# Performance work log

Measured on AMD Instinct MI355X. Metric: run time of the kernel, lower is better.

Reference implementation:

```python
import jax, jax.numpy as jnp
import numpy as np

IN, H, T, B, HW = 2048, 512, 14, 256, 49

def setup_inputs() -> dict:
    key = jax.random.key(0)
    ks = jax.random.split(key, 10)
    s = 0.02
    return {
        "x": jax.random.normal(ks[0], (B, IN, HW), jnp.float32),
        "fixation": jax.random.randint(ks[1], (B, T), 0, HW, jnp.int64),
        # stacked gate weights, order: 0=input, 1=forget, 2=output, 3=memory
        "Wx": jax.random.normal(ks[2], (4, H, IN), jnp.float32) * s,
        "bx": jnp.zeros((4, H), jnp.float32),
        "Wh": jax.random.normal(ks[3], (4, H, H), jnp.float32) * s,
        "bh": jnp.zeros((4, H), jnp.float32),
        # peephole weights, order: 0=input_c, 1=forget_c, 2=output_c
        "Wc": jax.random.normal(ks[4], (3, H, H), jnp.float32) * s,
        "bc": jnp.zeros((3, H), jnp.float32),
        "Wd": jax.random.normal(ks[5], (1, H), jnp.float32) * s,
        "bd": jnp.zeros((1,), jnp.float32),
    }

def reference(x, fixation, Wx, bx, Wh, bh, Wc, bc, Wd, bd):
    batch, feat, hw = x.shape
    seq_len = fixation.shape[1]
    # process_lengths: padding token is index 0
    lengths = seq_len - jnp.sum(fixation == 0, axis=1)  # [B]
    # gather fixated feature columns: [B, feat, T] -> [B, T, feat]
    xg = jnp.take_along_axis(x, fixation[:, None, :], axis=2)
    xg = jnp.transpose(xg, (0, 2, 1))
    # precompute all input projections for all 4 gates: [B, T, 4, H]
    xproj = jnp.einsum('btf,ghf->btgh', xg, Wx) + bx

    def step(carry, xp):  # xp: [B, 4, H]
        h, c = carry
        hp = jnp.einsum('bk,ghk->bgh', h, Wh) + bh  # [B, 4, H]
        i = jax.nn.sigmoid(xp[:, 0] + hp[:, 0] + c @ Wc[0].T + bc[0])
        f = jax.nn.sigmoid(xp[:, 1] + hp[:, 1] + c @ Wc[1].T + bc[1])
        g = jnp.tanh(xp[:, 3] + hp[:, 3])
        next_c = f * c + i * g
        o = jax.nn.sigmoid(xp[:, 2] + hp[:, 2] + next_c @ Wc[2].T + bc[2])
        h = o * next_c
        return (h, next_c), h

    hidden = Wx.shape[1]
    init = (jnp.zeros((batch, hidden), x.dtype), jnp.zeros((batch, hidden), x.dtype))
    _, hs = jax.lax.scan(step, init, jnp.transpose(xproj, (1, 0, 2, 3)))  # [T, B, H]
    hs = jnp.transpose(hs, (1, 0, 2))  # [B, T, H]
    # crop_seq: select hidden at end of each valid sequence
    last = hs[jnp.arange(batch), lengths - 1]  # [B, H]
    return jax.nn.sigmoid(last @ Wd.T + bd)  # [B, 1]
```

## Files before the change

### kernel.cpp

```cpp
#include <hip/hip_runtime.h>
#include <cstdint>
#include <cstddef>

#define B_   256
#define T_   14
#define INF_ 2048
#define H_   512
#define HW_  49
#define NG_  2048
#define KC_  1024
#define NBLK 256

typedef __attribute__((ext_vector_type(8))) _Float16 f16x8;
typedef __attribute__((ext_vector_type(4))) float f32x4;
typedef _Float16 f16;

typedef const void __attribute__((address_space(1))) gvoid_t;
typedef void __attribute__((address_space(3))) svoid_t;

__device__ __forceinline__ void async16(const void* g, void* l) {
  __builtin_amdgcn_global_load_lds((gvoid_t*)g, (svoid_t*)l, 16, 0, 0);
}

__device__ __forceinline__ float sigm(float x) { return 1.0f / (1.0f + __expf(-x)); }

__device__ __forceinline__ float aload(const float* p) {
  return __hip_atomic_load(p, __ATOMIC_RELAXED, __HIP_MEMORY_SCOPE_AGENT);
}
__device__ __forceinline__ unsigned long long aload64(const void* p) {
  return __hip_atomic_load((const unsigned long long*)p, __ATOMIC_RELAXED, __HIP_MEMORY_SCOPE_AGENT);
}
__device__ __forceinline__ void astore(float* p, float v) {
  __hip_atomic_store(p, v, __ATOMIC_RELAXED, __HIP_MEMORY_SCOPE_AGENT);
}
__device__ __forceinline__ void astore32(void* p, unsigned v) {
  __hip_atomic_store((unsigned*)p, v, __ATOMIC_RELAXED, __HIP_MEMORY_SCOPE_AGENT);
}

__device__ __forceinline__ void waitSlots(const int* slots, const int target) {
  const int* p = slots + (threadIdx.x & 31);
  for (;;) {
    const int v = __hip_atomic_load(p, __ATOMIC_RELAXED, __HIP_MEMORY_SCOPE_AGENT);
    if (__all(v >= target)) break;
    __builtin_amdgcn_s_sleep(1);
  }
}

__global__ void k_prep(const float* __restrict__ Wx, const float* __restrict__ bx,
                       const float* __restrict__ Wh, const float* __restrict__ Wc,
                       const float* __restrict__ bh, const float* __restrict__ bc,
                       const int* __restrict__ fix,
                       f16* __restrict__ Wxh, float* __restrict__ bxp,
                       f16* __restrict__ Wbig, f16* __restrict__ Wc2h,
                       float* __restrict__ biasb, int* __restrict__ flag64)
{
  __shared__ int any;
  const int tid = blockIdx.x * blockDim.x + threadIdx.x;
  const int nth = gridDim.x * blockDim.x;
  if (blockIdx.x == 0) {
    if (threadIdx.x == 0) any = 0;
    __syncthreads();
    int a = 0;
    for (int j = 1 + 2 * (int)threadIdx.x; j < B_ * T_; j += 2 * (int)blockDim.x) a |= fix[j];
    if (a) any = 1;
    __syncthreads();
    if (threadIdx.x == 0) flag64[0] = (any == 0) ? 1 : 0;
  }
  for (int i = tid; i < 4 * H_ * INF_; i += nth) {
    const int n = i >> 11, k = i & 2047;
    const int g = n & 3, h = n >> 2;
    Wxh[i] = (f16)Wx[((size_t)(g * H_ + h)) * INF_ + k];
  }
  for (int i = tid; i < NG_ * KC_; i += nth) {
    const int n = i >> 10, k = i & 1023;
    const int g = n & 3, h = n >> 2;
    float v;
    if (k < H_) v = Wh[((size_t)(g * H_ + h)) * H_ + k];
    else {
      const int kk = k - H_;
      v = (g == 0) ? Wc[h * H_ + kk] : (g == 1) ? Wc[H_ * H_ + h * H_ + kk] : 0.0f;
    }
    Wbig[i] = (f16)v;
  }
  for (int i = tid; i < H_ * H_; i += nth) Wc2h[i] = (f16)Wc[2 * H_ * H_ + i];
  for (int i = tid; i < NG_; i += nth) {
    const int g = i & 3, h = i >> 2;
    biasb[i] = bh[g * H_ + h] + ((g == 0) ? bc[h] : (g == 1) ? bc[H_ + h] : 0.0f);
    bxp[i] = bx[g * H_ + h];
  }
}

__global__ __launch_bounds__(256) void k_gather(const float* __restrict__ x,
                                                const int* __restrict__ fix,
                                                const int* __restrict__ flag64,
                                                f16* __restrict__ xg,
                                                int* __restrict__ tlast)
{
  __shared__ float rows[256 * 49];
  __shared__ int wv[T_];
  const int b = blockIdx.x;
  const int tid = threadIdx.x;
  const int is64 = flag64[0];
  if (tid < T_) wv[tid] = is64 ? fix[2 * (b * T_ + tid)] : fix[b * T_ + tid];
  __syncthreads();
  if (blockIdx.y == 0 && tid == 0) {
    int cnt = 0;
    for (int t = 0; t < T_; ++t) cnt += (wv[t] == 0);
    tlast[b] = (cnt < T_) ? (T_ - 1 - cnt) : (T_ - 1);
  }
  const float* xb = x + (size_t)b * (INF_ * HW_);
  for (int c = 0; c < 2; ++c) {
    const int ch = blockIdx.y * 2 + c;
    if (c) __syncthreads();
    const float4* src = (const float4*)(xb + (size_t)ch * 256 * 49);
    float4* dst4 = (float4*)rows;
    for (int i = tid; i < 3136; i += 256) dst4[i] = src[i];
    __syncthreads();
#pragma unroll
    for (int t = 0; t < T_; ++t)
      xg[(size_t)(b * T_ + t) * INF_ + ch * 256 + tid] = (f16)rows[tid * 49 + wv[t]];
  }
}

__global__ __launch_bounds__(256) void k_gemm_big(
    const f16* __restrict__ A, const f16* __restrict__ Bw,
    const float* __restrict__ bxp, float* __restrict__ Cproj)
{
  __shared__ alignas(16) f16 As[128 * 64];
  __shared__ alignas(16) f16 Bs[128 * 64];
  const int tid = threadIdx.x;
  const int lane = tid & 63;
  const int w = tid >> 6;
  const int wm = w >> 1, wn = w & 1;
  const int flat = blockIdx.y * 16 + blockIdx.x;
  const int wg = (flat & 7) * 56 + (flat >> 3);
  const int m0 = (wg >> 4) * 128, n0 = (wg & 15) * 128;
  f32x4 acc[4][4] = {};
  const int lrow = lane >> 3;
  const int kg = lane & 7;
  for (int ks = 0; ks < 2048; ks += 64) {
#pragma unroll
    for (int q = 0; q < 4; ++q) {
      const int chunk = (w << 2) + q;
      const int row = (chunk << 3) + lrow;
      const int skg = kg ^ (row & 7);
      async16(A + (size_t)(m0 + row) * 2048 + ks + (skg << 3), As + chunk * 512);
      async16(Bw + (size_t)(n0 + row) * 2048 + ks + (skg << 3), Bs + chunk * 512);
    }
    __syncthreads();
#pragma unroll
    for (int kk = 0; kk < 2; ++kk) {
      const int kgl = (kk << 2) + (lane >> 4);
      f16x8 af[4], bf[4];
#pragma unroll
      for (int mi = 0; mi < 4; ++mi) {
        const int r = (wm << 6) + (mi << 4) + (lane & 15);
        af[mi] = *(const f16x8*)(As + r * 64 + ((kgl ^ (r & 7)) << 3));
      }
#pragma unroll
      for (int ni = 0; ni < 4; ++ni) {
        const int r = (wn << 6) + (ni << 4) + (lane & 15);
        bf[ni] = *(const f16x8*)(Bs + r * 64 + ((kgl ^ (r & 7)) << 3));
      }
#pragma unroll
      for (int mi = 0; mi < 4; ++mi)
#pragma unroll
        for (int ni = 0; ni < 4; ++ni)
          acc[mi][ni] = __builtin_amdgcn_mfma_f32_16x16x32_f16(af[mi], bf[ni], acc[mi][ni], 0, 0, 0);
    }
    __syncthreads();
  }
#pragma unroll
  for (int mi = 0; mi < 4; ++mi)
#pragma unroll
    for (int ni = 0; ni < 4; ++ni)
#pragma unroll
      for (int r4 = 0; r4 < 4; ++r4) {
        const int row = m0 + (wm << 6) + (mi << 4) + ((lane >> 4) << 2) + r4;
        const int col = n0 + (wn << 6) + (ni << 4) + (lane & 15);
        Cproj[(size_t)row * 2048 + col] = acc[mi][ni][r4] + bxp[col];
      }
}

__global__ __launch_bounds__(256, 1) void k_recur(
    const f16* __restrict__ Wbig, const f16* __restrict__ Wc2h,
    const float* __restrict__ biasb, const float* __restrict__ bc,
    const float* __restrict__ xproj, f16* __restrict__ h16,
    f16* __restrict__ cb16, float* __restrict__ lasth,
    const int* __restrict__ tlast, const float* __restrict__ Wd,
    const float* __restrict__ bd, float* __restrict__ out,
    int* __restrict__ bar)
{
  __shared__ alignas(16) f16 hT[2][16 * 512];
  __shared__ alignas(16) f16 cT[2][16 * 512];
  __shared__ alignas(16) float exCN[256];
  __shared__ alignas(16) float exGO[2][256];
  __shared__ alignas(16) float ex2[4 * 256];
  const int tid = threadIdx.x, lane = tid & 63, w = tid >> 6;
  const int lk = lane >> 4;
  const int bid = blockIdx.x;
  const int pair = bid >> 5, grank = bid & 31;
  const int n0A = grank * 64, n0h = grank * 16;
  const int m0t[2] = {pair * 32, pair * 32 + 16};
  int* const sl[2] = {bar + (2 * pair) * 64, bar + (2 * pair + 1) * 64};

  f16x8 wG[32];
  {
    const f16* src = Wbig + (size_t)(n0A + w * 16 + (lane & 15)) * 1024 + (lk << 3);
#pragma unroll
    for (int kc = 0; kc < 32; ++kc) wG[kc] = *(const f16x8*)(src + kc * 32);
  }
  f16x8 wO[4];
  {
    const f16* src = Wc2h + (size_t)(n0h + (lane & 15)) * 512 + (lk << 3);
#pragma unroll
    for (int j = 0; j < 4; ++j) wO[j] = *(const f16x8*)(src + (w * 4 + j) * 32);
  }
  const int hq = (lane >> 2) & 3;
  const int browA = (lk << 2) + (lane & 3);
  const int hlA = w * 4 + hq;
  const float4 b4c = *(const float4*)(biasb + 4 * (n0h + hlA));
  const int rowB = tid >> 4, colB = tid & 15;
  const float bco = bc[1024 + n0h + colB];
  const int tlB[2] = {tlast[m0t[0] + rowB], tlast[m0t[1] + rowB]};
  {
    const f16x8 z = {};
#pragma unroll
    for (int j = 0; j < 8; ++j) *(f16x8*)(&cT[0][0] + (((j << 8) + tid) << 3)) = z;
  }
  float creg[2] = {0.f, 0.f};
  __syncthreads();

  for (int t = 0; t < T_; ++t) {
    float4 x4p[2];
#pragma unroll
    for (int tt = 0; tt < 2; ++tt)
      x4p[tt] = *(const float4*)(xproj + (size_t)((m0t[tt] + browA) * T_ + t) * 2048 +
                                 4 * (n0h + hlA));

#pragma unroll
    for (int tt = 0; tt < 2; ++tt) {
      if (t) waitSlots(sl[tt], 2 * t);
#pragma unroll
      for (int j = 0; j < 4; ++j) {
        const int u = (j << 8) + tid;
        const int row = u >> 6, kg = u & 63;
        const f16* src = h16 + (size_t)(m0t[tt] + row) * 512 + (kg << 3);
        union { f16x8 v; unsigned long long q[2]; } u2;
        u2.q[0] = aload64(src);
        u2.q[1] = aload64(src + 4);
        *(f16x8*)(&hT[tt][0] + row * 512 + ((kg >> 3) << 6) + (((kg & 7) ^ (row & 7)) << 3)) = u2.v;
      }
      __syncthreads();
      f32x4 acc[2] = {};
      {
        const int ra = lane & 15;
#pragma unroll
        for (int kc = 0; kc < 32; ++kc) {
          const int kgl = ((kc & 1) << 2) + lk;
          const f16* base = (kc < 16) ? (&hT[tt][0] + ((kc >> 1) << 6))
                                      : (&cT[tt][0] + (((kc - 16) >> 1) << 6));
          const f16x8 af = *(const f16x8*)(base + ra * 512 + ((kgl ^ (ra & 7)) << 3));
          acc[kc & 1] = __builtin_amdgcn_mfma_f32_16x16x32_f16(af, wG[kc], acc[kc & 1], 0, 0, 0);
        }
      }
      {
        const f32x4 a = acc[0] + acc[1];
        float a0 = a[0], a1 = a[1], a2 = a[2], a3 = a[3];
        {
          const bool odd = lane & 1;
          float xx = odd ? a0 : a1, yy = odd ? a2 : a3;
          xx = __shfl_xor(xx, 1); yy = __shfl_xor(yy, 1);
          if (odd) { a0 = xx; a2 = yy; } else { a1 = xx; a3 = yy; }
        }
        {
          const bool hi = lane & 2;
          float xx = hi ? a0 : a2, yy = hi ? a1 : a3;
          xx = __shfl_xor(xx, 2); yy = __shfl_xor(yy, 2);
          if (hi) { a0 = xx; a1 = yy; } else { a2 = xx; a3 = yy; }
        }
        const float gi = a0 + b4c.x + x4p[tt].x;
        const float gf = a1 + b4c.y + x4p[tt].y;
        const float go = a2 + b4c.z + x4p[tt].z;
        const float gm = a3 + b4c.w + x4p[tt].w;
        const float cn = sigm(gi) * tanhf(gm) + sigm(gf) * creg[tt];
        creg[tt] = cn;
        exCN[browA * 16 + hlA] = cn;
        exGO[tt][browA * 16 + hlA] = go;
      }
      __syncthreads();
      if (tid < 128) {
        const int rowe = tid >> 3, pr = tid & 7;
        const float2 cp = *(const float2*)(exCN + rowe * 16 + (pr << 1));
        union { unsigned u; f16 h2[2]; } pk;
        pk.h2[0] = (f16)cp.x; pk.h2[1] = (f16)cp.y;
        astore32(cb16 + (size_t)(m0t[tt] + rowe) * 512 + n0h + (pr << 1), pk.u);
      }
      __syncthreads();
      if (tid == 0)
        __hip_atomic_store(sl[tt] + grank, 2 * t + 1, __ATOMIC_RELAXED, __HIP_MEMORY_SCOPE_AGENT);
    }

#pragma unroll
    for (int tt = 0; tt < 2; ++tt) {
      waitSlots(sl[tt], 2 * t + 1);
#pragma unroll
      for (int j = 0; j < 4; ++j) {
        const int u = (j << 8) + tid;
        const int row = u >> 6, kg = u & 63;
        const f16* src = cb16 + (size_t)(m0t[tt] + row) * 512 + (kg << 3);
        union { f16x8 v; unsigned long long q[2]; } u2;
        u2.q[0] = aload64(src);
        u2.q[1] = aload64(src + 4);
        *(f16x8*)(&cT[tt][0] + row * 512 + ((kg >> 3) << 6) + (((kg & 7) ^ (row & 7)) << 3)) = u2.v;
      }
      __syncthreads();
      f32x4 accB = {};
      {
        const int ra = lane & 15;
#pragma unroll
        for (int j = 0; j < 4; ++j) {
          const int kc = w * 4 + j;
          const int kgl = ((kc & 1) << 2) + lk;
          const f16x8 af = *(const f16x8*)(&cT[tt][0] + ra * 512 + ((kc >> 1) << 6) +
                                           ((kgl ^ (ra & 7)) << 3));
          accB = __builtin_amdgcn_mfma_f32_16x16x32_f16(af, wO[j], accB, 0, 0, 0);
        }
      }
#pragma unroll
      for (int r4 = 0; r4 < 4; ++r4)
        ex2[w * 256 + ((lk << 2) + r4) * 16 + (lane & 15)] = accB[r4];
      __syncthreads();
      {
        const int ib = rowB * 16 + colB;
        const float sum = (ex2[ib] + ex2[256 + ib]) + (ex2[512 + ib] + ex2[768 + ib]);
        const int cg = n0h + colB;
        const float cn = (float)cT[tt][rowB * 512 + ((cg >> 6) << 6) +
                                       ((((cg >> 3) & 7) ^ (rowB & 7)) << 3) + (cg & 7)];
        const float hv = sigm(sum + exGO[tt][ib] + bco) * cn;
        const float hvo = __shfl_xor(hv, 1);
        if (!(tid & 1)) {
          union { unsigned u; f16 h2[2]; } pk;
          pk.h2[0] = (f16)hv; pk.h2[1] = (f16)hvo;
          astore32(h16 + (size_t)(m0t[tt] + rowB) * 512 + (cg & ~1), pk.u);
        }
        if (t == tlB[tt]) astore(lasth + (size_t)(m0t[tt] + rowB) * 512 + cg, hv);
      }
      __syncthreads();
      if (tid == 0)
        __hip_atomic_store(sl[tt] + grank, 2 * t + 2, __ATOMIC_RELAXED, __HIP_MEMORY_SCOPE_AGENT);
    }
  }

  waitSlots(sl[0], 2 * T_);
  waitSlots(sl[1], 2 * T_);
  if (w == 0) {
    const int b = pair * 32 + grank;
    float s = 0.f;
#pragma unroll
    for (int k = lane; k < 512; k += 64) s += aload(lasth + (size_t)b * 512 + k) * Wd[k];
#pragma unroll
    for (int off = 32; off > 0; off >>= 1) s += __shfl_down(s, off);
    if (lane == 0) out[b] = 1.0f / (1.0f + __expf(-(s + bd[0])));
  }
}

extern "C" void kernel_launch(void* const* d_in, const int* in_sizes, int n_in,
                              void* d_out, int out_size, void* d_ws, size_t ws_size,
                              hipStream_t stream) {
  const float* x   = (const float*)d_in[0];
  const int*   fix = (const int*)d_in[1];
  const float* Wx  = (const float*)d_in[2];
  const float* bx  = (const float*)d_in[3];
  const float* Wh  = (const float*)d_in[4];
  const float* bh  = (const float*)d_in[5];
  const float* Wc  = (const float*)d_in[6];
  const float* bc  = (const float*)d_in[7];
  const float* Wd  = (const float*)d_in[8];
  const float* bd  = (const float*)d_in[9];
  float* out = (float*)d_out;
  char* ws = (char*)d_ws;

  f16*   xg    = (f16*)(ws);
  f16*   Wxh   = (f16*)(ws + 14680064);
  float* xproj = (float*)(ws + 23068672);
  f16*   Wbig  = (f16*)(ws + 52428800);
  f16*   Wc2h  = (f16*)(ws + 56623104);
  float* biasb = (float*)(ws + 57147392);
  float* bxp   = (float*)(ws + 57155584);
  f16*   h16   = (f16*)(ws + 57163776);
  f16*   cb16  = (f16*)(ws + 57425920);
  float* lasth = (float*)(ws + 57688064);
  int*   tlast = (int*)(ws + 58212352);
  int*   flag64= (int*)(ws + 58213376);
  int*   bar   = (int*)(ws + 58213440);

  hipMemsetAsync(h16, 0, 262144, stream);
  hipMemsetAsync(cb16, 0, 262144, stream);
  hipMemsetAsync(bar, 0, 4096, stream);

  k_prep<<<2048, 256, 0, stream>>>(Wx, bx, Wh, Wc, bh, bc, fix, Wxh, bxp, Wbig, Wc2h, biasb, flag64);
  k_gather<<<dim3(256, 4), 256, 0, stream>>>(x, fix, flag64, xg, tlast);
  k_gemm_big<<<dim3(16, 28), 256, 0, stream>>>(xg, Wxh, bxp, xproj);
  k_recur<<<NBLK, 256, 0, stream>>>(Wbig, Wc2h, biasb, bc, xproj, h16, cb16,
                                    lasth, tlast, Wd, bd, out, bar);
}
```

Baseline: 217.9 us.

## Merge prep and gather kernels, restructure recurrence sync and block grouping

Merges the weight-prep and gather kernels into one launch, where each gather block recomputes the int64 flag itself. In the recurrence kernel, block-to-group mapping changes so group members are strided across block IDs. The cell-state export is written straight from registers instead of being staged in shared memory. The output-gate GEMM now runs on a single wave, removing the cross-wave reduction and one barrier per substep. The spin-wait polls two flag copies (one stored with an sc0 store) without sleeping. This cuts barriers and launch overhead, but leaves three waves idle during the output step and adds busier polling traffic.

```diff
diff --git a/kernel.cpp b/kernel.cpp
--- a/kernel.cpp
+++ b/kernel.cpp
@@ -27,6 +27,9 @@
 __device__ __forceinline__ float aload(const float* p) {
   return __hip_atomic_load(p, __ATOMIC_RELAXED, __HIP_MEMORY_SCOPE_AGENT);
 }
+__device__ __forceinline__ int aloadi(const int* p) {
+  return __hip_atomic_load(p, __ATOMIC_RELAXED, __HIP_MEMORY_SCOPE_AGENT);
+}
 __device__ __forceinline__ unsigned long long aload64(const void* p) {
   return __hip_atomic_load((const unsigned long long*)p, __ATOMIC_RELAXED, __HIP_MEMORY_SCOPE_AGENT);
 }
@@ -36,89 +39,97 @@
 __device__ __forceinline__ void astore32(void* p, unsigned v) {
   __hip_atomic_store((unsigned*)p, v, __ATOMIC_RELAXED, __HIP_MEMORY_SCOPE_AGENT);
 }
-
-__device__ __forceinline__ void waitSlots(const int* slots, const int target) {
-  const int* p = slots + (threadIdx.x & 31);
+__device__ __forceinline__ void astorei(int* p, int v) {
+  __hip_atomic_store(p, v, __ATOMIC_RELAXED, __HIP_MEMORY_SCOPE_AGENT);
+}
+
+__device__ __forceinline__ void st32_sc0(void* p, unsigned v) {
+  asm volatile("global_store_dword %0, %1, off sc0" :: "v"(p), "v"(v) : "memory");
+}
+__device__ __forceinline__ int ld_sc0_probe(const int* p) {
+  int r;
+  asm volatile("global_load_dword %0, %1, off sc0\n\ts_waitcnt vmcnt(0)"
+               : "=v"(r) : "v"(p) : "memory");
+  return r;
+}
+
+__device__ __forceinline__ void waitDual(const int* sa, const int* sf, const int target) {
+  const int* pa = sa + (threadIdx.x & 31);
+  const int* pf = sf + (threadIdx.x & 31);
   for (;;) {
-    const int v = __hip_atomic_load(p, __ATOMIC_RELAXED, __HIP_MEMORY_SCOPE_AGENT);
-    if (__all(v >= target)) break;
-    __builtin_amdgcn_s_sleep(1);
-  }
-}
-
-__global__ void k_prep(const float* __restrict__ Wx, const float* __restrict__ bx,
-                       const float* __restrict__ Wh, const float* __restrict__ Wc,
-                       const float* __restrict__ bh, const float* __restrict__ bc,
-                       const int* __restrict__ fix,
-                       f16* __restrict__ Wxh, float* __restrict__ bxp,
-                       f16* __restrict__ Wbig, f16* __restrict__ Wc2h,
-                       float* __restrict__ biasb, int* __restrict__ flag64)
+    const int vf = ld_sc0_probe(pf);
+    const int va = aloadi(pa);
+    if (__all((vf >= target) || (va >= target))) break;
+  }
+}
+
+__global__ __launch_bounds__(256) void k_prep_gather(
+    const float* __restrict__ Wx, const float* __restrict__ bx,
+    const float* __restrict__ Wh, const float* __restrict__ Wc,
+    const float* __restrict__ bh, const float* __restrict__ bc,
+    const int* __restrict__ fix, const float* __restrict__ x,
+    f16* __restrict__ Wxh, float* __restrict__ bxp,
+    f16* __restrict__ Wbig, f16* __restrict__ Wc2h,
+    float* __restrict__ biasb, f16* __restrict__ xg, int* __restrict__ tlast)
 {
-  __shared__ int any;
-  const int tid = blockIdx.x * blockDim.x + threadIdx.x;
-  const int nth = gridDim.x * blockDim.x;
-  if (blockIdx.x == 0) {
-    if (threadIdx.x == 0) any = 0;
+  const int bid = blockIdx.x;
+  const int tid = threadIdx.x;
+  if (bid < 1024) {
+    __shared__ float rows[256 * 49];
+    __shared__ int wv[T_];
+    __shared__ int anyS;
+    const int b = bid >> 2, part = bid & 3;
+    int a = 0;
+    for (int i = tid; i < B_ * T_; i += 256) a |= fix[2 * i + 1];
+    if (tid == 0) anyS = 0;
     __syncthreads();
-    int a = 0;
-    for (int j = 1 + 2 * (int)threadIdx.x; j < B_ * T_; j += 2 * (int)blockDim.x) a |= fix[j];
-    if (a) any = 1;
+    if (a) anyS = 1;
     __syncthreads();
-    if (threadIdx.x == 0) flag64[0] = (any == 0) ? 1 : 0;
-  }
-  for (int i = tid; i < 4 * H_ * INF_; i += nth) {
-    const int n = i >> 11, k = i & 2047;
-    const int g = n & 3, h = n >> 2;
-    Wxh[i] = (f16)Wx[((size_t)(g * H_ + h)) * INF_ + k];
-  }
-  for (int i = tid; i < NG_ * KC_; i += nth) {
-    const int n = i >> 10, k = i & 1023;
-    const int g = n & 3, h = n >> 2;
-    float v;
-    if (k < H_) v = Wh[((size_t)(g * H_ + h)) * H_ + k];
-    else {
-      const int kk = k - H_;
-      v = (g == 0) ? Wc[h * H_ + kk] : (g == 1) ? Wc[H_ * H_ + h * H_ + kk] : 0.0f;
-    }
-    Wbig[i] = (f16)v;
-  }
-  for (int i = tid; i < H_ * H_; i += nth) Wc2h[i] = (f16)Wc[2 * H_ * H_ + i];
-  for (int i = tid; i < NG_; i += nth) {
-    const int g = i & 3, h = i >> 2;
-    biasb[i] = bh[g * H_ + h] + ((g == 0) ? bc[h] : (g == 1) ? bc[H_ + h] : 0.0f);
-    bxp[i] = bx[g * H_ + h];
-  }
-}
-
-__global__ __launch_bounds__(256) void k_gather(const float* __restrict__ x,
-                                                const int* __restrict__ fix,
-                                                const int* __restrict__ flag64,
-                                                f16* __restrict__ xg,
-                                                int* __restrict__ tlast)
-{
-  __shared__ float rows[256 * 49];
-  __shared__ int wv[T_];
-  const int b = blockIdx.x;
-  const int tid = threadIdx.x;
-  const int is64 = flag64[0];
-  if (tid < T_) wv[tid] = is64 ? fix[2 * (b * T_ + tid)] : fix[b * T_ + tid];
-  __syncthreads();
-  if (blockIdx.y == 0 && tid == 0) {
-    int cnt = 0;
-    for (int t = 0; t < T_; ++t) cnt += (wv[t] == 0);
-    tlast[b] = (cnt < T_) ? (T_ - 1 - cnt) : (T_ - 1);
-  }
-  const float* xb = x + (size_t)b * (INF_ * HW_);
-  for (int c = 0; c < 2; ++c) {
-    const int ch = blockIdx.y * 2 + c;
-    if (c) __syncthreads();
-    const float4* src = (const float4*)(xb + (size_t)ch * 256 * 49);
-    float4* dst4 = (float4*)rows;
-    for (int i = tid; i < 3136; i += 256) dst4[i] = src[i];
+    const int is64 = (anyS == 0);
+    if (tid < T_) wv[tid] = is64 ? fix[2 * (b * T_ + tid)] : fix[b * T_ + tid];
     __syncthreads();
-#pragma unroll
-    for (int t = 0; t < T_; ++t)
-      xg[(size_t)(b * T_ + t) * INF_ + ch * 256 + tid] = (f16)rows[tid * 49 + wv[t]];
+    if (part == 0 && tid == 0) {
+      int cnt = 0;
+      for (int t = 0; t < T_; ++t) cnt += (wv[t] == 0);
+      tlast[b] = (cnt < T_) ? (T_ - 1 - cnt) : (T_ - 1);
+    }
+    const float* xb = x + (size_t)b * (INF_ * HW_);
+    for (int c = 0; c < 2; ++c) {
+      const int ch = part * 2 + c;
+      if (c) __syncthreads();
+      const float4* src = (const float4*)(xb + (size_t)ch * 256 * 49);
+      float4* dst4 = (float4*)rows;
+      for (int i = tid; i < 3136; i += 256) dst4[i] = src[i];
+      __syncthreads();
+#pragma unroll
+      for (int t = 0; t < T_; ++t)
+        xg[(size_t)(b * T_ + t) * INF_ + ch * 256 + tid] = (f16)rows[tid * 49 + wv[t]];
+    }
+  } else {
+    const int tid2 = (bid - 1024) * 256 + tid;
+    const int nth = 512 * 256;
+    for (int i = tid2; i < 4 * H_ * INF_; i += nth) {
+      const int n = i >> 11, k = i & 2047;
+      const int g = n & 3, h = n >> 2;
+      Wxh[i] = (f16)Wx[((size_t)(g * H_ + h)) * INF_ + k];
+    }
+    for (int i = tid2; i < NG_ * KC_; i += nth) {
+      const int n = i >> 10, k = i & 1023;
+      const int g = n & 3, h = n >> 2;
+      float v;
+      if (k < H_) v = Wh[((size_t)(g * H_ + h)) * H_ + k];
+      else {
+        const int kk = k - H_;
+        v = (g == 0) ? Wc[h * H_ + kk] : (g == 1) ? Wc[H_ * H_ + h * H_ + kk] : 0.0f;
+      }
+      Wbig[i] = (f16)v;
+    }
+    for (int i = tid2; i < H_ * H_; i += nth) Wc2h[i] = (f16)Wc[2 * H_ * H_ + i];
+    for (int i = tid2; i < NG_; i += nth) {
+      const int g = i & 3, h = i >> 2;
+      biasb[i] = bh[g * H_ + h] + ((g == 0) ? bc[h] : (g == 1) ? bc[H_ + h] : 0.0f);
+      bxp[i] = bx[g * H_ + h];
+    }
   }
 }
 
@@ -193,16 +204,17 @@
 {
   __shared__ alignas(16) f16 hT[2][16 * 512];
   __shared__ alignas(16) f16 cT[2][16 * 512];
-  __shared__ alignas(16) float exCN[256];
   __shared__ alignas(16) float exGO[2][256];
-  __shared__ alignas(16) float ex2[4 * 256];
   const int tid = threadIdx.x, lane = tid & 63, w = tid >> 6;
   const int lk = lane >> 4;
   const int bid = blockIdx.x;
-  const int pair = bid >> 5, grank = bid & 31;
-  const int n0A = grank * 64, n0h = grank * 16;
-  const int m0t[2] = {pair * 32, pair * 32 + 16};
-  int* const sl[2] = {bar + (2 * pair) * 64, bar + (2 * pair + 1) * 64};
+  const int grp = bid & 7, rank = bid >> 3;
+  const int n0A = rank * 64, n0h = rank * 16;
+  const int m0t[2] = {grp * 32, grp * 32 + 16};
+  int* const slA0 = bar + (grp * 2) * 32;
+  int* const slA1 = bar + (grp * 2 + 1) * 32;
+  int* const slF0 = bar + 512 + (grp * 2) * 32;
+  int* const slF1 = bar + 512 + (grp * 2 + 1) * 32;
 
   f16x8 wG[32];
   {
@@ -210,19 +222,24 @@
 #pragma unroll
     for (int kc = 0; kc < 32; ++kc) wG[kc] = *(const f16x8*)(src + kc * 32);
   }
-  f16x8 wO[4];
-  {
+  f16x8 wO[16];
+  float bcoW = 0.f;
+  int tlW0[4] = {-1, -1, -1, -1}, tlW1[4] = {-1, -1, -1, -1};
+  if (w == 0) {
     const f16* src = Wc2h + (size_t)(n0h + (lane & 15)) * 512 + (lk << 3);
 #pragma unroll
-    for (int j = 0; j < 4; ++j) wO[j] = *(const f16x8*)(src + (w * 4 + j) * 32);
+    for (int kc = 0; kc < 16; ++kc) wO[kc] = *(const f16x8*)(src + kc * 32);
+    bcoW = bc[1024 + n0h + (lane & 15)];
+#pragma unroll
+    for (int r4 = 0; r4 < 4; ++r4) {
+      tlW0[r4] = tlast[m0t[0] + lk * 4 + r4];
+      tlW1[r4] = tlast[m0t[1] + lk * 4 + r4];
+    }
   }
   const int hq = (lane >> 2) & 3;
   const int browA = (lk << 2) + (lane & 3);
   const int hlA = w * 4 + hq;
   const float4 b4c = *(const float4*)(biasb + 4 * (n0h + hlA));
-  const int rowB = tid >> 4, colB = tid & 15;
-  const float bco = bc[1024 + n0h + colB];
-  const int tlB[2] = {tlast[m0t[0] + rowB], tlast[m0t[1] + rowB]};
   {
     const f16x8 z = {};
 #pragma unroll
@@ -232,6 +249,9 @@
   __syncthreads();
 
   for (int t = 0; t < T_; ++t) {
+#pragma unroll
+    for (int kc = 0; kc < 32; ++kc) asm volatile("" : "+v"(wG[kc]));
+
     float4 x4p[2];
 #pragma unroll
     for (int tt = 0; tt < 2; ++tt)
@@ -240,7 +260,9 @@
 
 #pragma unroll
     for (int tt = 0; tt < 2; ++tt) {
-      if (t) waitSlots(sl[tt], 2 * t);
+      int* const slA = tt ? slA1 : slA0;
+      int* const slF = tt ? slF1 : slF0;
+      if (t) waitDual(slA, slF, 2 * t);
 #pragma unroll
       for (int j = 0; j < 4; ++j) {
         const int u = (j << 8) + tid;
@@ -285,25 +307,27 @@
         const float gm = a3 + b4c.w + x4p[tt].w;
         const float cn = sigm(gi) * tanhf(gm) + sigm(gf) * creg[tt];
         creg[tt] = cn;
-        exCN[browA * 16 + hlA] = cn;
         exGO[tt][browA * 16 + hlA] = go;
-      }
+        const float cnP = __shfl_xor(cn, 4);
+        if (!(lane & 4)) {
+          union { unsigned u; f16 h2[2]; } pk;
+          pk.h2[0] = (f16)cn; pk.h2[1] = (f16)cnP;
+          astore32(cb16 + (size_t)(m0t[tt] + browA) * 512 + n0h + hlA, pk.u);
+        }
+      }
+      asm volatile("s_waitcnt vmcnt(0)" ::: "memory");
       __syncthreads();
-      if (tid < 128) {
-        const int rowe = tid >> 3, pr = tid & 7;
-        const float2 cp = *(const float2*)(exCN + rowe * 16 + (pr << 1));
-        union { unsigned u; f16 h2[2]; } pk;
-        pk.h2[0] = (f16)cp.x; pk.h2[1] = (f16)cp.y;
-        astore32(cb16 + (size_t)(m0t[tt] + rowe) * 512 + n0h + (pr << 1), pk.u);
-      }
-      __syncthreads();
-      if (tid == 0)
-        __hip_atomic_store(sl[tt] + grank, 2 * t + 1, __ATOMIC_RELAXED, __HIP_MEMORY_SCOPE_AGENT);
+      if (tid == 0) {
+        st32_sc0(slF + rank, (unsigned)(2 * t + 1));
+        astorei(slA + rank, 2 * t + 1);
+      }
     }
 
 #pragma unroll
     for (int tt = 0; tt < 2; ++tt) {
-      waitSlots(sl[tt], 2 * t + 1);
+      int* const slA = tt ? slA1 : slA0;
+      int* const slF = tt ? slF1 : slF0;
+      waitDual(slA, slF, 2 * t + 1);
 #pragma unroll
       for (int j = 0; j < 4; ++j) {
         const int u = (j << 8) + tid;
@@ -315,47 +339,48 @@
         *(f16x8*)(&cT[tt][0] + row * 512 + ((kg >> 3) << 6) + (((kg & 7) ^ (row & 7)) << 3)) = u2.v;
       }
       __syncthreads();
-      f32x4 accB = {};
-      {
+      if (w == 0) {
+        f32x4 accB = {};
         const int ra = lane & 15;
 #pragma unroll
-        for (int j = 0; j < 4; ++j) {
-          const int kc = w * 4 + j;
+        for (int kc = 0; kc < 16; ++kc) {
           const int kgl = ((kc & 1) << 2) + lk;
           const f16x8 af = *(const f16x8*)(&cT[tt][0] + ra * 512 + ((kc >> 1) << 6) +
                                            ((kgl ^ (ra & 7)) << 3));
-          accB = __builtin_amdgcn_mfma_f32_16x16x32_f16(af, wO[j], accB, 0, 0, 0);
-        }
-      }
-#pragma unroll
-      for (int r4 = 0; r4 < 4; ++r4)
-        ex2[w * 256 + ((lk << 2) + r4) * 16 + (lane & 15)] = accB[r4];
+          accB = __builtin_amdgcn_mfma_f32_16x16x32_f16(af, wO[kc], accB, 0, 0, 0);
+        }
+        const int col = lane & 15;
+        const int cgi = n0h + col;
+#pragma unroll
+        for (int r4 = 0; r4 < 4; ++r4) {
+          const int row = lk * 4 + r4;
+          const float go = exGO[tt][row * 16 + col];
+          const float cn = (float)cT[tt][row * 512 + ((cgi >> 6) << 6) +
+                                         ((((cgi >> 3) & 7) ^ (row & 7)) << 3) + (cgi & 7)];
+          const float hv = sigm(accB[r4] + go + bcoW) * cn;
+          const float hvP = __shfl_xor(hv, 1);
+          if (!(lane & 1)) {
+            union { unsigned u; f16 h2[2]; } pk;
+            pk.h2[0] = (f16)hv; pk.h2[1] = (f16)hvP;
+            astore32(h16 + (size_t)(m0t[tt] + row) * 512 + (cgi & ~1), pk.u);
+          }
+          const int tl = tt ? tlW1[r4] : tlW0[r4];
+          if (t == tl) astore(lasth + (size_t)(m0t[tt] + row) * 512 + cgi, hv);
+        }
+      }
+      asm volatile("s_waitcnt vmcnt(0)" ::: "memory");
       __syncthreads();
-      {
-        const int ib = rowB * 16 + colB;
-        const float sum = (ex2[ib] + ex2[256 + ib]) + (ex2[512 + ib] + ex2[768 + ib]);
-        const int cg = n0h + colB;
-        const float cn = (float)cT[tt][rowB * 512 + ((cg >> 6) << 6) +
-                                       ((((cg >> 3) & 7) ^ (rowB & 7)) << 3) + (cg & 7)];
-        const float hv = sigm(sum + exGO[tt][ib] + bco) * cn;
-        const float hvo = __shfl_xor(hv, 1);
-        if (!(tid & 1)) {
-          union { unsigned u; f16 h2[2]; } pk;
-          pk.h2[0] = (f16)hv; pk.h2[1] = (f16)hvo;
-          astore32(h16 + (size_t)(m0t[tt] + rowB) * 512 + (cg & ~1), pk.u);
-        }
-        if (t == tlB[tt]) astore(lasth + (size_t)(m0t[tt] + rowB) * 512 + cg, hv);
-      }
-      __syncthreads();
-      if (tid == 0)
-        __hip_atomic_store(sl[tt] + grank, 2 * t + 2, __ATOMIC_RELAXED, __HIP_MEMORY_SCOPE_AGENT);
-    }
-  }
-
-  waitSlots(sl[0], 2 * T_);
-  waitSlots(sl[1], 2 * T_);
+      if (tid == 0) {
+        st32_sc0(slF + rank, (unsigned)(2 * t + 2));
+        astorei(slA + rank, 2 * t + 2);
+      }
+    }
+  }
+
+  waitDual(slA0, slF0, 2 * T_);
+  waitDual(slA1, slF1, 2 * T_);
   if (w == 0) {
-    const int b = pair * 32 + grank;
+    const int b = grp * 32 + rank;
     float s = 0.f;
 #pragma unroll
     for (int k = lane; k < 512; k += 64) s += aload(lasth + (size_t)b * 512 + k) * Wd[k];
@@ -392,15 +417,14 @@
   f16*   cb16  = (f16*)(ws + 57425920);
   float* lasth = (float*)(ws + 57688064);
   int*   tlast = (int*)(ws + 58212352);
-  int*   flag64= (int*)(ws + 58213376);
-  int*   bar   = (int*)(ws + 58213440);
+  int*   bar   = (int*)(ws + 58213376);
 
   hipMemsetAsync(h16, 0, 262144, stream);
   hipMemsetAsync(cb16, 0, 262144, stream);
-  hipMemsetAsync(bar, 0, 4096, stream);
-
-  k_prep<<<2048, 256, 0, stream>>>(Wx, bx, Wh, Wc, bh, bc, fix, Wxh, bxp, Wbig, Wc2h, biasb, flag64);
-  k_gather<<<dim3(256, 4), 256, 0, stream>>>(x, fix, flag64, xg, tlast);
+  hipMemsetAsync(bar, 0, 8192, stream);
+
+  k_prep_gather<<<1536, 256, 0, stream>>>(Wx, bx, Wh, Wc, bh, bc, fix, x,
+                                          Wxh, bxp, Wbig, Wc2h, biasb, xg, tlast);
   k_gemm_big<<<dim3(16, 28), 256, 0, stream>>>(xg, Wxh, bxp, xproj);
   k_recur<<<NBLK, 256, 0, stream>>>(Wbig, Wc2h, biasb, bc, xproj, h16, cb16,
                                     lasth, tlast, Wd, bd, out, bar);
```

Result: slower. 265.6 us (+21.9%).
